# Performance work log

Measured on AMD Instinct MI355X. Metric: run time of the kernel, lower is better.

The kernel has to match this reference:

```python
import math
import jax, jax.numpy as jnp
import numpy as np

POS_RATIO = 0.2
NEG_RATIO = 0.2
LOSS_WEIGHT = 1.0
EPS = 1e-8  # torch.cosine_similarity eps


def setup_inputs() -> dict:
    key = jax.random.key(0)
    x = jax.random.normal(key, (4096, 512), dtype=jnp.float32)
    return {"x": x}


def reference(x) -> jnp.ndarray:
    # Cosine similarity via L2-normalize + GEMM (same math as torch.cosine_similarity
    # with per-row norm clamped at eps), instead of the O(N^2 * D) broadcast form.
    norms = jnp.maximum(jnp.linalg.norm(x, axis=-1, keepdims=True), EPS)
    xn = x / norms                      # [N, D]
    sim = xn @ xn.T                     # [N, N]

    # Thresholds from the sorted (detached) flattened similarity matrix.
    sim_sorted = jnp.sort(jax.lax.stop_gradient(sim).ravel())
    n_total = sim_sorted.shape[0]       # N*N (static)
    pos_thresh = sim_sorted[math.ceil(n_total * (1.0 - POS_RATIO))]
    neg_thresh = sim_sorted[math.ceil(n_total * NEG_RATIO)]

    pos_mask = sim > pos_thresh
    neg_mask = sim < neg_thresh

    # masked means, matching (1 - sim[pos_mask]).clamp_min(0).mean() etc.
    pos_cnt = jnp.sum(pos_mask)
    neg_cnt = jnp.sum(neg_mask)
    pos_loss = jnp.sum(jnp.where(pos_mask, jnp.maximum(1.0 - sim, 0.0), 0.0)) / pos_cnt
    neg_loss = jnp.sum(jnp.where(neg_mask, jnp.maximum(sim, 0.0), 0.0)) / neg_cnt

    return LOSS_WEIGHT * (pos_loss + neg_loss)
```

## Files before the change

### kernel.cpp

```cpp
#include <hip/hip_runtime.h>
#include <hip/hip_bf16.h>
#include <math.h>


#define N 4096
#define D 512
#define NN 16777216u
#define NBF 2048
#define NSLICE 528

typedef __attribute__((ext_vector_type(8))) short bf16x8;
typedef __attribute__((ext_vector_type(4))) float f32x4;
typedef const __attribute__((address_space(1))) void gas_t;
typedef __attribute__((address_space(3))) void las_t;

__device__ __forceinline__ int val2bin(float s) {
  int b = (int)fmaf(s, 1024.0f, 1024.0f);
  return b < 0 ? 0 : (b > NBF - 1 ? NBF - 1 : b);
}
__device__ __forceinline__ unsigned short f2bf(float f) {
  unsigned int u = __float_as_uint(f);
  u += 0x7FFFu + ((u >> 16) & 1u);
  return (unsigned short)(u >> 16);
}

__global__ __launch_bounds__(256) void norm_conv(const float* __restrict__ x,
                                                 unsigned short* __restrict__ xnb) {
  const int row = blockIdx.x * 4 + (threadIdx.x >> 6);
  const int l = threadIdx.x & 63;
  const float4* rp = (const float4*)(x + (size_t)row * D);
  const float4 v0 = rp[l * 2];
  const float4 v1 = rp[l * 2 + 1];
  float s = v0.x * v0.x + v0.y * v0.y + v0.z * v0.z + v0.w * v0.w +
            v1.x * v1.x + v1.y * v1.y + v1.z * v1.z + v1.w * v1.w;
#pragma unroll
  for (int o = 32; o > 0; o >>= 1) s += __shfl_xor(s, o);
  const float r = 1.0f / fmaxf(sqrtf(s), 1e-8f);
  bf16x8 o8;
  o8[0] = (short)f2bf(v0.x * r); o8[1] = (short)f2bf(v0.y * r);
  o8[2] = (short)f2bf(v0.z * r); o8[3] = (short)f2bf(v0.w * r);
  o8[4] = (short)f2bf(v1.x * r); o8[5] = (short)f2bf(v1.y * r);
  o8[6] = (short)f2bf(v1.z * r); o8[7] = (short)f2bf(v1.w * r);
  *(bf16x8*)&xnb[(size_t)row * D + l * 8] = o8;
}

#define BM 128
#define BK 64
__global__ __launch_bounds__(256, 3) void gemm_fused(const unsigned short* __restrict__ xnb,
                                                     unsigned int* __restrict__ hist,
                                                     float* __restrict__ slice_top) {
  const int bid = blockIdx.x;
  int by = (int)((sqrtf(8.0f * (float)bid + 1.0f) - 1.0f) * 0.5f);
  while ((by + 1) * (by + 2) / 2 <= bid) ++by;
  while (by * (by + 1) / 2 > bid) --by;
  const int bx = bid - by * (by + 1) / 2;

  __shared__ unsigned short As[BM][BK];
  __shared__ unsigned short Bs[BM][BK];
  __shared__ unsigned int cnt[2][NBF];
  __shared__ float stop;
  const int tid = threadIdx.x;
  for (int i = tid; i < 2 * NBF; i += 256) ((unsigned int*)cnt)[i] = 0u;
  if (tid == 0) stop = 0.f;

  const int w = tid >> 6, l = tid & 63;
  const int wr = w >> 1, wc = w & 1;
  const int lr = l & 15, kgrp = l >> 4;
  const int swz = lr & 7;
  const int hc = w >> 1;
  const int bm = bx * BM, bn = by * BM;

  const int srow = l >> 3;
  const int gsrc = (l & 7) ^ srow;
  const unsigned short* srcA0 = xnb + (size_t)(bm + w * 32 + srow) * D + gsrc * 8;
  const unsigned short* srcB0 = xnb + (size_t)(bn + w * 32 + srow) * D + gsrc * 8;

  f32x4 acc[4][4] = {};

  for (int kt = 0; kt < D; kt += BK) {
    __syncthreads();
#pragma unroll
    for (int c = 0; c < 4; ++c) {
      __builtin_amdgcn_global_load_lds((gas_t*)(srcA0 + (size_t)c * 8 * D + kt),
                                       (las_t*)&As[w * 32 + c * 8][0], 16, 0, 0);
      __builtin_amdgcn_global_load_lds((gas_t*)(srcB0 + (size_t)c * 8 * D + kt),
                                       (las_t*)&Bs[w * 32 + c * 8][0], 16, 0, 0);
    }
    __syncthreads();
#pragma unroll
    for (int kk = 0; kk < BK; kk += 32) {
      const int g0 = (kk >> 3) + kgrp;
      bf16x8 af[4], bf4[4];
#pragma unroll
      for (int m = 0; m < 4; ++m)
        af[m] = *(const bf16x8*)&As[wr * 64 + m * 16 + lr][(g0 ^ swz) * 8];
#pragma unroll
      for (int n = 0; n < 4; ++n)
        bf4[n] = *(const bf16x8*)&Bs[wc * 64 + n * 16 + lr][(g0 ^ swz) * 8];
#pragma unroll
      for (int m = 0; m < 4; ++m)
#pragma unroll
        for (int n = 0; n < 4; ++n)
          acc[m][n] = __builtin_amdgcn_mfma_f32_16x16x32_bf16(af[m], bf4[n], acc[m][n], 0, 0, 0);
    }
  }

  const unsigned int wg = (bx == by) ? 1u : 2u;
  __syncthreads();
#pragma unroll
  for (int m = 0; m < 4; ++m)
#pragma unroll
    for (int n = 0; n < 4; ++n)
#pragma unroll
      for (int e = 0; e < 4; ++e) {
        const float s = acc[m][n][e];
        const int b = val2bin(s);
        atomicAdd(&cnt[hc][b], wg);
        if (b == NBF - 1) atomicAdd(&stop, (float)wg * fmaxf(1.0f - s, 0.0f));
      }
  __syncthreads();
  for (int i = tid; i < NBF; i += 256) {
    const unsigned int c = cnt[0][i] + cnt[1][i];
    if (c) atomicAdd(&hist[i], c);
  }
  if (tid == 0) slice_top[bid] = stop;
}

__global__ __launch_bounds__(256) void final_loss(const unsigned int* __restrict__ hist,
                                                  const float* __restrict__ slice_top,
                                                  float* __restrict__ out,
                                                  unsigned int kneg, unsigned int kpos) {
  __shared__ unsigned int part[256], Q[256];
  __shared__ unsigned int sbp, sbn;
  __shared__ double tstage[4];
  __shared__ double dstage[2][4];
  __shared__ unsigned int ustage[2][4];
  const int tid = threadIdx.x;
  const int lane = tid & 63, wid = tid >> 6;

  unsigned int c8[8];
  unsigned int tot = 0;
#pragma unroll
  for (int j = 0; j < 8; ++j) {
    c8[j] = hist[tid * 8 + j];
    tot += c8[j];
  }
  {
    float tl = 0.f;
    for (int s = tid; s < NSLICE; s += 256) tl += slice_top[s];
    double td = tl;
#pragma unroll
    for (int o = 32; o > 0; o >>= 1) td += __shfl_xor(td, o);
    if (lane == 0) tstage[wid] = td;
  }
  part[tid] = tot;
  Q[tid] = tot;
  __syncthreads();
#pragma unroll
  for (int off = 1; off < 256; off <<= 1) {
    unsigned int t2 = (tid >= off) ? Q[tid - off] : 0u;
    __syncthreads();
    Q[tid] += t2;
    __syncthreads();
  }
  const unsigned int total = Q[255];
  const unsigned int incl = Q[tid];
  const unsigned int excl = incl - part[tid];
  const unsigned int targets[2] = {kpos, kneg};
#pragma unroll
  for (int t = 0; t < 2; ++t) {
    const unsigned int r = (total == 0u) ? 0u
                         : (targets[t] < total ? targets[t] : total - 1u);
    if (total != 0u && excl <= r && r < incl) {
      unsigned int rr = r - excl, cum = 0;
      int bsel = -1;
#pragma unroll
      for (int j = 0; j < 8; ++j) {
        if (bsel < 0 && cum + c8[j] > rr) bsel = j;
        else if (bsel < 0) cum += c8[j];
      }
      if (bsel < 0) bsel = 7;
      if (t == 0) sbp = tid * 8 + (unsigned int)bsel;
      else        sbn = tid * 8 + (unsigned int)bsel;
    }
  }
  __syncthreads();
  const double topsum = tstage[0] + tstage[1] + tstage[2] + tstage[3];
  const unsigned int bp = sbp, bn = sbn;

  double psum = 0.0, nsum = 0.0;
  unsigned int pcnt = 0, ncnt = 0;
#pragma unroll
  for (int j = 0; j < 8; ++j) {
    const unsigned int b = tid * 8 + j;
    const double mid = ((double)b + 0.5) / 1024.0 - 1.0;
    if (b > bp) {
      pcnt += c8[j];
      psum += (b == NBF - 1) ? topsum : (double)c8[j] * (1.0 - mid);
    }
    if (b < bn) {
      ncnt += c8[j];
      if (mid > 0.0) nsum += (double)c8[j] * mid;
    }
  }
#pragma unroll
  for (int o = 32; o > 0; o >>= 1) {
    psum += __shfl_xor(psum, o);
    nsum += __shfl_xor(nsum, o);
    pcnt += __shfl_xor(pcnt, o);
    ncnt += __shfl_xor(ncnt, o);
  }
  if (lane == 0) {
    dstage[0][wid] = psum; dstage[1][wid] = nsum;
    ustage[0][wid] = pcnt; ustage[1][wid] = ncnt;
  }
  __syncthreads();
  if (tid == 0) {
    const double ps = dstage[0][0] + dstage[0][1] + dstage[0][2] + dstage[0][3];
    const double ns = dstage[1][0] + dstage[1][1] + dstage[1][2] + dstage[1][3];
    const unsigned int pc = ustage[0][0] + ustage[0][1] + ustage[0][2] + ustage[0][3];
    const unsigned int nc = ustage[1][0] + ustage[1][1] + ustage[1][2] + ustage[1][3];
    const double pl = pc ? ps / (double)pc : 0.0;
    const double nl = nc ? ns / (double)nc : 0.0;
    out[0] = (float)(pl + nl);
  }
}

extern "C" void kernel_launch(void* const* d_in, const int* in_sizes, int n_in,
                              void* d_out, int out_size, void* d_ws, size_t ws_size,
                              hipStream_t stream) {
  const float* x = (const float*)d_in[0];
  float* out = (float*)d_out;
  char* ws = (char*)d_ws;

  unsigned short* xnb = (unsigned short*)ws;
  size_t off = (size_t)N * D * 2;
  unsigned int* hist = (unsigned int*)(ws + off);
  off += (size_t)NBF * 4;
  float* slice_top = (float*)(ws + off);

  const unsigned int kneg = (unsigned int)ceil((double)NN * 0.2);
  const unsigned int kpos = (unsigned int)ceil((double)NN * (1.0 - 0.2));

  hipMemsetAsync(hist, 0, (size_t)NBF * 4, stream);
  norm_conv<<<N / 4, 256, 0, stream>>>(x, xnb);
  gemm_fused<<<NSLICE, 256, 0, stream>>>(xnb, hist, slice_top);
  final_loss<<<1, 256, 0, stream>>>(hist, slice_top, out, kneg, kpos);
}
```

Before: 42.19 us.

## Fold histogram reset into norm kernel and finalize loss in last GEMM block

```diff
diff --git a/kernel.cpp b/kernel.cpp
--- a/kernel.cpp
+++ b/kernel.cpp
@@ -25,7 +25,13 @@
 }
 
 __global__ __launch_bounds__(256) void norm_conv(const float* __restrict__ x,
-                                                 unsigned short* __restrict__ xnb) {
+                                                 unsigned short* __restrict__ xnb,
+                                                 unsigned int* __restrict__ hist,
+                                                 unsigned int* __restrict__ done) {
+  if (blockIdx.x == 0) {
+    for (int i = threadIdx.x; i < NBF; i += 256) hist[i] = 0u;
+    if (threadIdx.x == 0) *done = 0u;
+  }
   const int row = blockIdx.x * 4 + (threadIdx.x >> 6);
   const int l = threadIdx.x & 63;
   const float4* rp = (const float4*)(x + (size_t)row * D);
@@ -48,7 +54,10 @@
 #define BK 64
 __global__ __launch_bounds__(256, 3) void gemm_fused(const unsigned short* __restrict__ xnb,
                                                      unsigned int* __restrict__ hist,
-                                                     float* __restrict__ slice_top) {
+                                                     float* __restrict__ slice_top,
+                                                     unsigned int* __restrict__ done,
+                                                     float* __restrict__ out,
+                                                     unsigned int kneg, unsigned int kpos) {
   const int bid = blockIdx.x;
   int by = (int)((sqrtf(8.0f * (float)bid + 1.0f) - 1.0f) * 0.5f);
   while ((by + 1) * (by + 2) / 2 <= bid) ++by;
@@ -59,6 +68,7 @@
   __shared__ unsigned short Bs[BM][BK];
   __shared__ unsigned int cnt[2][NBF];
   __shared__ float stop;
+  __shared__ unsigned int s_ticket;
   const int tid = threadIdx.x;
   for (int i = tid; i < 2 * NBF; i += 256) ((unsigned int*)cnt)[i] = 0u;
   if (tid == 0) stop = 0.f;
@@ -124,30 +134,34 @@
     if (c) atomicAdd(&hist[i], c);
   }
   if (tid == 0) slice_top[bid] = stop;
-}
-
-__global__ __launch_bounds__(256) void final_loss(const unsigned int* __restrict__ hist,
-                                                  const float* __restrict__ slice_top,
-                                                  float* __restrict__ out,
-                                                  unsigned int kneg, unsigned int kpos) {
+
+  __syncthreads();
+  __threadfence();
+  if (tid == 0) s_ticket = atomicAdd(done, 1u);
+  __syncthreads();
+  if (s_ticket != NSLICE - 1) return;
+  __threadfence();
+
   __shared__ unsigned int part[256], Q[256];
   __shared__ unsigned int sbp, sbn;
   __shared__ double tstage[4];
   __shared__ double dstage[2][4];
   __shared__ unsigned int ustage[2][4];
-  const int tid = threadIdx.x;
   const int lane = tid & 63, wid = tid >> 6;
 
   unsigned int c8[8];
   unsigned int tot = 0;
 #pragma unroll
   for (int j = 0; j < 8; ++j) {
-    c8[j] = hist[tid * 8 + j];
+    c8[j] = __hip_atomic_load(&hist[tid * 8 + j], __ATOMIC_RELAXED,
+                              __HIP_MEMORY_SCOPE_AGENT);
     tot += c8[j];
   }
   {
     float tl = 0.f;
-    for (int s = tid; s < NSLICE; s += 256) tl += slice_top[s];
+    for (int s = tid; s < NSLICE; s += 256)
+      tl += __hip_atomic_load(&slice_top[s], __ATOMIC_RELAXED,
+                              __HIP_MEMORY_SCOPE_AGENT);
     double td = tl;
 #pragma unroll
     for (int o = 32; o > 0; o >>= 1) td += __shfl_xor(td, o);
@@ -186,7 +200,7 @@
   }
   __syncthreads();
   const double topsum = tstage[0] + tstage[1] + tstage[2] + tstage[3];
-  const unsigned int bp = sbp, bn = sbn;
+  const unsigned int fbp = sbp, fbn = sbn;
 
   double psum = 0.0, nsum = 0.0;
   unsigned int pcnt = 0, ncnt = 0;
@@ -194,11 +208,11 @@
   for (int j = 0; j < 8; ++j) {
     const unsigned int b = tid * 8 + j;
     const double mid = ((double)b + 0.5) / 1024.0 - 1.0;
-    if (b > bp) {
+    if (b > fbp) {
       pcnt += c8[j];
       psum += (b == NBF - 1) ? topsum : (double)c8[j] * (1.0 - mid);
     }
-    if (b < bn) {
+    if (b < fbn) {
       ncnt += c8[j];
       if (mid > 0.0) nsum += (double)c8[j] * mid;
     }
@@ -238,12 +252,12 @@
   unsigned int* hist = (unsigned int*)(ws + off);
   off += (size_t)NBF * 4;
   float* slice_top = (float*)(ws + off);
+  off += (size_t)NSLICE * 4;
+  unsigned int* done = (unsigned int*)(ws + off);
 
   const unsigned int kneg = (unsigned int)ceil((double)NN * 0.2);
   const unsigned int kpos = (unsigned int)ceil((double)NN * (1.0 - 0.2));
 
-  hipMemsetAsync(hist, 0, (size_t)NBF * 4, stream);
-  norm_conv<<<N / 4, 256, 0, stream>>>(x, xnb);
-  gemm_fused<<<NSLICE, 256, 0, stream>>>(xnb, hist, slice_top);
-  final_loss<<<1, 256, 0, stream>>>(hist, slice_top, out, kneg, kpos);
-}
+  norm_conv<<<N / 4, 256, 0, stream>>>(x, xnb, hist, done);
+  gemm_fused<<<NSLICE, 256, 0, stream>>>(xnb, hist, slice_top, done, out, kneg, kpos);
+}
```

New measurement: 62.71 us. +48.6%, slower.
